# Performance work log

Measured on AMD Instinct MI355X. Metric: run time of the kernel, lower is better.

## Reference

```python
import jax, jax.numpy as jnp
import numpy as np

B, N, F_IN = 8, 1024, 128
C, E_FEAT, H = 128, 64, 4
E = 32768
NEG_SLOPE = 0.2


def setup_inputs() -> dict:
    key = jax.random.key(0)
    ks = jax.random.split(key, 7)
    return {
        "src": jax.random.normal(ks[0], (B, N, F_IN), dtype=jnp.float32),
        "edge_index": jax.random.randint(ks[1], (2, E), 0, N, dtype=jnp.int32),
        "W_lin": jax.random.normal(ks[2], (F_IN, C), dtype=jnp.float32) * (1.0 / np.sqrt(F_IN)),
        "a_src": jax.random.normal(ks[3], (C, H), dtype=jnp.float32) * (1.0 / np.sqrt(C)),
        "a_dst": jax.random.normal(ks[4], (C, H), dtype=jnp.float32) * (1.0 / np.sqrt(C)),
        "W_edge": jax.random.normal(ks[5], (F_IN, E_FEAT), dtype=jnp.float32) * (1.0 / np.sqrt(F_IN)),
        "a_edge": jax.random.normal(ks[6], (E_FEAT, H), dtype=jnp.float32) * (1.0 / np.sqrt(E_FEAT)),
    }


def reference(src, edge_index, W_lin, a_src, a_dst, W_edge, a_edge):
    # src: [B,N,F_in]; edge_index: [2,E]
    b, n, _ = src.shape
    h = a_src.shape[1]
    x = jnp.einsum("bnf,fc->bnc", src, W_lin)            # [B,N,C]
    attn_src = jnp.einsum("bnc,ch->bnh", x, a_src)        # [B,N,H]
    attn_dst = jnp.einsum("bnc,ch->bnh", x, a_dst)        # [B,N,H]
    # attn[b,i,j,h] = attn_src[b,i,h] + attn_dst[b,j,h]
    attn = attn_src[:, :, None, :] + attn_dst[:, None, :, :]  # [B,N,N,H]
    # edge term: (src_i - src_j) -> lin_edge -> a_edge, scattered into dense [B,N,N,H]
    diff = src[:, edge_index[0], :] - src[:, edge_index[1], :]    # [B,E,F_in]
    evals = jnp.einsum("bef,fd,dh->beh", diff, W_edge, a_edge)    # [B,E,H]
    edge_dense = jnp.zeros((b, n, n, h), src.dtype).at[:, edge_index[0], edge_index[1], :].add(evals)
    attn = jax.nn.leaky_relu(attn + edge_dense, NEG_SLOPE)
    # source applies softmax over the last dim (heads), faithful to nn.Softmax(dim=-1)
    return jax.nn.softmax(attn, axis=-1)
```

## Files before the change

kernel.cpp:

```cpp
#include <hip/hip_runtime.h>

#define B_SZ 8
#define N_SZ 1024
#define F_IN 128
#define C_DIM 128
#define E_FEAT 64
#define H_SZ 4
#define E_NUM 32768
#define NEG_SLOPE 0.2f


__global__ __launch_bounds__(256) void fold_mats(
    const float* __restrict__ W_lin, const float* __restrict__ a_src,
    const float* __restrict__ a_dst, const float* __restrict__ W_edge,
    const float* __restrict__ a_edge,
    float* __restrict__ m_src, float* __restrict__ m_dst,
    float* __restrict__ m_edge) {
  int idx = blockIdx.x * blockDim.x + threadIdx.x;
  if (idx >= F_IN * H_SZ) return;
  int f = idx >> 2, h = idx & 3;
  float accs = 0.f, accd = 0.f;
  for (int c = 0; c < C_DIM; ++c) {
    float w = W_lin[f * C_DIM + c];
    accs += w * a_src[c * H_SZ + h];
    accd += w * a_dst[c * H_SZ + h];
  }
  float acce = 0.f;
  for (int d = 0; d < E_FEAT; ++d)
    acce += W_edge[f * E_FEAT + d] * a_edge[d * H_SZ + h];
  m_src[idx] = accs; m_dst[idx] = accd; m_edge[idx] = acce;
}

__global__ __launch_bounds__(256) void node_vecs(
    const float* __restrict__ src, const float* __restrict__ m_src,
    const float* __restrict__ m_dst, const float* __restrict__ m_edge,
    float* __restrict__ as_, float* __restrict__ ad_, float* __restrict__ sw_) {
  int tid = blockIdx.x * blockDim.x + threadIdx.x;
  int h = tid & 3;
  int bn = tid >> 2;
  const float* row = src + (size_t)bn * F_IN;
  float a = 0.f, d = 0.f, e = 0.f;
  for (int f = 0; f < F_IN; ++f) {
    float s = row[f];
    a += s * m_src[f * H_SZ + h];
    d += s * m_dst[f * H_SZ + h];
    e += s * m_edge[f * H_SZ + h];
  }
  as_[tid] = a; ad_[tid] = d; sw_[tid] = e;
}

__global__ __launch_bounds__(256) void count_edges(
    const int* __restrict__ ei, int* __restrict__ cnt) {
  int e = blockIdx.x * blockDim.x + threadIdx.x;
  if (e < E_NUM) atomicAdd(&cnt[ei[e]], 1);
}

__global__ __launch_bounds__(1024) void scan_counts(
    const int* __restrict__ cnt, int* __restrict__ excl,
    int* __restrict__ cursor) {
  __shared__ int s[N_SZ];
  int t = threadIdx.x;
  int v0 = cnt[t];
  s[t] = v0;
  __syncthreads();
  for (int d = 1; d < N_SZ; d <<= 1) {
    int v = (t >= d) ? s[t - d] : 0;
    __syncthreads();
    s[t] += v;
    __syncthreads();
  }
  int ex = s[t] - v0;
  excl[t] = ex;
  cursor[t] = ex;
}

__global__ __launch_bounds__(256) void fill_edges(
    const int* __restrict__ ei, int* __restrict__ cursor,
    int* __restrict__ ebuf) {
  int e = blockIdx.x * blockDim.x + threadIdx.x;
  if (e >= E_NUM) return;
  int i = ei[e];
  int j = ei[E_NUM + e];
  int pos = atomicAdd(&cursor[i], 1);
  ebuf[pos] = j;
}

__global__ __launch_bounds__(256) void attn_main(
    const float* __restrict__ as_, const float* __restrict__ ad_,
    const float* __restrict__ sw_, const int* __restrict__ cnt,
    const int* __restrict__ excl, const int* __restrict__ ebuf,
    float* __restrict__ out) {
  __shared__ float row[N_SZ * H_SZ];
  int i = blockIdx.x, b = blockIdx.y, t = threadIdx.x;

  float4* row4 = (float4*)row;
  for (int k = t; k < N_SZ; k += 256) row4[k] = make_float4(0.f, 0.f, 0.f, 0.f);

  const float4* sw4 = (const float4*)sw_;
  float4 swi = sw4[b * N_SZ + i];
  float4 asi = ((const float4*)as_)[b * N_SZ + i];
  __syncthreads();

  int off = excl[i], c = cnt[i];
  for (int k = t; k < c; k += 256) {
    int j = ebuf[off + k];
    float4 swj = sw4[b * N_SZ + j];
    atomicAdd(&row[j * 4 + 0], swi.x - swj.x);
    atomicAdd(&row[j * 4 + 1], swi.y - swj.y);
    atomicAdd(&row[j * 4 + 2], swi.z - swj.z);
    atomicAdd(&row[j * 4 + 3], swi.w - swj.w);
  }
  __syncthreads();

  const float4* ad4 = (const float4*)ad_;
  float4* out4 = (float4*)out + (size_t)(b * N_SZ + i) * N_SZ;
#pragma unroll
  for (int r = 0; r < 4; ++r) {
    int j = r * 256 + t;
    float4 adj = ad4[b * N_SZ + j];
    float4 rv = row4[j];
    float v0 = asi.x + adj.x + rv.x;
    float v1 = asi.y + adj.y + rv.y;
    float v2 = asi.z + adj.z + rv.z;
    float v3 = asi.w + adj.w + rv.w;
    v0 = v0 > 0.f ? v0 : v0 * NEG_SLOPE;
    v1 = v1 > 0.f ? v1 : v1 * NEG_SLOPE;
    v2 = v2 > 0.f ? v2 : v2 * NEG_SLOPE;
    v3 = v3 > 0.f ? v3 : v3 * NEG_SLOPE;
    float m = fmaxf(fmaxf(v0, v1), fmaxf(v2, v3));
    float e0 = __expf(v0 - m);
    float e1 = __expf(v1 - m);
    float e2 = __expf(v2 - m);
    float e3 = __expf(v3 - m);
    float inv = 1.f / (e0 + e1 + e2 + e3);
    out4[j] = make_float4(e0 * inv, e1 * inv, e2 * inv, e3 * inv);
  }
}

extern "C" void kernel_launch(void* const* d_in, const int* in_sizes, int n_in,
                              void* d_out, int out_size, void* d_ws,
                              size_t ws_size, hipStream_t stream) {
  const float* src    = (const float*)d_in[0];
  const int*   ei     = (const int*)d_in[1];
  const float* W_lin  = (const float*)d_in[2];
  const float* a_src  = (const float*)d_in[3];
  const float* a_dst  = (const float*)d_in[4];
  const float* W_edge = (const float*)d_in[5];
  const float* a_edge = (const float*)d_in[6];
  float* out = (float*)d_out;

  float* ws     = (float*)d_ws;
  float* m_src  = ws;
  float* m_dst  = ws + 512;
  float* m_edge = ws + 1024;
  float* as_    = ws + 1536;
  float* ad_    = as_ + B_SZ * N_SZ * H_SZ;
  float* sw_    = ad_ + B_SZ * N_SZ * H_SZ;
  int*   cnt    = (int*)(sw_ + B_SZ * N_SZ * H_SZ);
  int*   excl   = cnt + N_SZ;
  int*   cursor = excl + N_SZ;
  int*   ebuf   = cursor + N_SZ;

  hipMemsetAsync(cnt, 0, N_SZ * sizeof(int), stream);
  count_edges<<<E_NUM / 256, 256, 0, stream>>>(ei, cnt);
  scan_counts<<<1, 1024, 0, stream>>>(cnt, excl, cursor);
  fill_edges<<<E_NUM / 256, 256, 0, stream>>>(ei, cursor, ebuf);
  fold_mats<<<2, 256, 0, stream>>>(W_lin, a_src, a_dst, W_edge, a_edge,
                                   m_src, m_dst, m_edge);
  node_vecs<<<B_SZ * N_SZ * H_SZ / 256, 256, 0, stream>>>(
      src, m_src, m_dst, m_edge, as_, ad_, sw_);
  attn_main<<<dim3(N_SZ, B_SZ), 256, 0, stream>>>(as_, ad_, sw_, cnt, excl,
                                                  ebuf, out);
}
```

Baseline: 190.3 us.

## Fuse prep kernels, warp-reduce node projections, seed row with ad, nontemporal stores

Folds the memset, edge count, scan, fill and fold-matrix launches into one two-block prep kernel that uses shared-memory atomics, cutting launch count from seven to three. The node projection kernel now has one wavefront per row and reduces with shuffles instead of a serial per-thread loop. The attention kernel seeds its shared row with ad instead of zeros, which removes a global load in the epilogue, and writes output with nontemporal stores. The cost is that the edge CSR build now runs serially in a single block.

```diff
diff --git a/kernel.cpp b/kernel.cpp
--- a/kernel.cpp
+++ b/kernel.cpp
@@ -9,80 +9,102 @@
 #define E_NUM 32768
 #define NEG_SLOPE 0.2f
 
+typedef float f4_t __attribute__((ext_vector_type(4)));
 
-__global__ __launch_bounds__(256) void fold_mats(
-    const float* __restrict__ W_lin, const float* __restrict__ a_src,
-    const float* __restrict__ a_dst, const float* __restrict__ W_edge,
-    const float* __restrict__ a_edge,
+
+__global__ __launch_bounds__(1024) void prep_kernel(
+    const int* __restrict__ ei, const float* __restrict__ W_lin,
+    const float* __restrict__ a_src, const float* __restrict__ a_dst,
+    const float* __restrict__ W_edge, const float* __restrict__ a_edge,
     float* __restrict__ m_src, float* __restrict__ m_dst,
-    float* __restrict__ m_edge) {
-  int idx = blockIdx.x * blockDim.x + threadIdx.x;
-  if (idx >= F_IN * H_SZ) return;
-  int f = idx >> 2, h = idx & 3;
-  float accs = 0.f, accd = 0.f;
-  for (int c = 0; c < C_DIM; ++c) {
-    float w = W_lin[f * C_DIM + c];
-    accs += w * a_src[c * H_SZ + h];
-    accd += w * a_dst[c * H_SZ + h];
+    float* __restrict__ m_edge, int* __restrict__ cnt_g,
+    int* __restrict__ excl_g, int* __restrict__ ebuf) {
+  if (blockIdx.x == 0) {
+    __shared__ int cntS[N_SZ];
+    __shared__ int s[N_SZ];
+    __shared__ int cur[N_SZ];
+    int t = threadIdx.x;
+    cntS[t] = 0;
+    __syncthreads();
+    for (int e = t; e < E_NUM; e += 1024) atomicAdd(&cntS[ei[e]], 1);
+    __syncthreads();
+    int v0 = cntS[t];
+    s[t] = v0;
+    __syncthreads();
+    for (int d2 = 1; d2 < N_SZ; d2 <<= 1) {
+      int v = (t >= d2) ? s[t - d2] : 0;
+      __syncthreads();
+      s[t] += v;
+      __syncthreads();
+    }
+    int ex = s[t] - v0;
+    cnt_g[t] = v0;
+    excl_g[t] = ex;
+    cur[t] = ex;
+    __syncthreads();
+    for (int e = t; e < E_NUM; e += 1024) {
+      int i = ei[e];
+      int j = ei[E_NUM + e];
+      int pos = atomicAdd(&cur[i], 1);
+      ebuf[pos] = j;
+    }
+  } else {
+    int idx = threadIdx.x;
+    if (idx >= F_IN * H_SZ) return;
+    int f = idx >> 2, h = idx & 3;
+    float accs = 0.f, accd = 0.f;
+    for (int c = 0; c < C_DIM; ++c) {
+      float w = W_lin[f * C_DIM + c];
+      accs += w * a_src[c * H_SZ + h];
+      accd += w * a_dst[c * H_SZ + h];
+    }
+    float acce = 0.f;
+    for (int d = 0; d < E_FEAT; ++d)
+      acce += W_edge[f * E_FEAT + d] * a_edge[d * H_SZ + h];
+    m_src[idx] = accs;
+    m_dst[idx] = accd;
+    m_edge[idx] = acce;
   }
-  float acce = 0.f;
-  for (int d = 0; d < E_FEAT; ++d)
-    acce += W_edge[f * E_FEAT + d] * a_edge[d * H_SZ + h];
-  m_src[idx] = accs; m_dst[idx] = accd; m_edge[idx] = acce;
 }
 
-__global__ __launch_bounds__(256) void node_vecs(
+__global__ __launch_bounds__(256) void nodes_kernel(
     const float* __restrict__ src, const float* __restrict__ m_src,
     const float* __restrict__ m_dst, const float* __restrict__ m_edge,
     float* __restrict__ as_, float* __restrict__ ad_, float* __restrict__ sw_) {
-  int tid = blockIdx.x * blockDim.x + threadIdx.x;
-  int h = tid & 3;
-  int bn = tid >> 2;
-  const float* row = src + (size_t)bn * F_IN;
-  float a = 0.f, d = 0.f, e = 0.f;
-  for (int f = 0; f < F_IN; ++f) {
-    float s = row[f];
-    a += s * m_src[f * H_SZ + h];
-    d += s * m_dst[f * H_SZ + h];
-    e += s * m_edge[f * H_SZ + h];
+  int wid = threadIdx.x >> 6, lane = threadIdx.x & 63;
+  int rid = blockIdx.x * 4 + wid;
+  const float* rp = src + (size_t)rid * F_IN;
+  float x0 = rp[lane];
+  float x1 = rp[lane + 64];
+  const float4* ms4 = (const float4*)m_src;
+  const float4* md4 = (const float4*)m_dst;
+  const float4* me4 = (const float4*)m_edge;
+  float4 s0 = ms4[lane], s1 = ms4[lane + 64];
+  float4 d0 = md4[lane], d1 = md4[lane + 64];
+  float4 e0 = me4[lane], e1 = me4[lane + 64];
+  float acc[12];
+  acc[0] = x0 * s0.x + x1 * s1.x;
+  acc[1] = x0 * s0.y + x1 * s1.y;
+  acc[2] = x0 * s0.z + x1 * s1.z;
+  acc[3] = x0 * s0.w + x1 * s1.w;
+  acc[4] = x0 * d0.x + x1 * d1.x;
+  acc[5] = x0 * d0.y + x1 * d1.y;
+  acc[6] = x0 * d0.z + x1 * d1.z;
+  acc[7] = x0 * d0.w + x1 * d1.w;
+  acc[8] = x0 * e0.x + x1 * e1.x;
+  acc[9] = x0 * e0.y + x1 * e1.y;
+  acc[10] = x0 * e0.z + x1 * e1.z;
+  acc[11] = x0 * e0.w + x1 * e1.w;
+#pragma unroll
+  for (int m = 1; m < 64; m <<= 1) {
+#pragma unroll
+    for (int q = 0; q < 12; ++q) acc[q] += __shfl_xor(acc[q], m);
   }
-  as_[tid] = a; ad_[tid] = d; sw_[tid] = e;
-}
-
-__global__ __launch_bounds__(256) void count_edges(
-    const int* __restrict__ ei, int* __restrict__ cnt) {
-  int e = blockIdx.x * blockDim.x + threadIdx.x;
-  if (e < E_NUM) atomicAdd(&cnt[ei[e]], 1);
-}
-
-__global__ __launch_bounds__(1024) void scan_counts(
-    const int* __restrict__ cnt, int* __restrict__ excl,
-    int* __restrict__ cursor) {
-  __shared__ int s[N_SZ];
-  int t = threadIdx.x;
-  int v0 = cnt[t];
-  s[t] = v0;
-  __syncthreads();
-  for (int d = 1; d < N_SZ; d <<= 1) {
-    int v = (t >= d) ? s[t - d] : 0;
-    __syncthreads();
-    s[t] += v;
-    __syncthreads();
+  if (lane == 0) {
+    ((float4*)as_)[rid] = make_float4(acc[0], acc[1], acc[2], acc[3]);
+    ((float4*)ad_)[rid] = make_float4(acc[4], acc[5], acc[6], acc[7]);
+    ((float4*)sw_)[rid] = make_float4(acc[8], acc[9], acc[10], acc[11]);
   }
-  int ex = s[t] - v0;
-  excl[t] = ex;
-  cursor[t] = ex;
-}
-
-__global__ __launch_bounds__(256) void fill_edges(
-    const int* __restrict__ ei, int* __restrict__ cursor,
-    int* __restrict__ ebuf) {
-  int e = blockIdx.x * blockDim.x + threadIdx.x;
-  if (e >= E_NUM) return;
-  int i = ei[e];
-  int j = ei[E_NUM + e];
-  int pos = atomicAdd(&cursor[i], 1);
-  ebuf[pos] = j;
 }
 
 __global__ __launch_bounds__(256) void attn_main(
@@ -92,19 +114,21 @@
     float* __restrict__ out) {
   __shared__ float row[N_SZ * H_SZ];
   int i = blockIdx.x, b = blockIdx.y, t = threadIdx.x;
+  int bN = b * N_SZ;
 
   float4* row4 = (float4*)row;
-  for (int k = t; k < N_SZ; k += 256) row4[k] = make_float4(0.f, 0.f, 0.f, 0.f);
+  const float4* ad4 = (const float4*)ad_;
+  const float4* sw4 = (const float4*)sw_;
+  for (int j = t; j < N_SZ; j += 256) row4[j] = ad4[bN + j];
 
-  const float4* sw4 = (const float4*)sw_;
-  float4 swi = sw4[b * N_SZ + i];
-  float4 asi = ((const float4*)as_)[b * N_SZ + i];
+  float4 swi = sw4[bN + i];
+  float4 asi = ((const float4*)as_)[bN + i];
   __syncthreads();
 
   int off = excl[i], c = cnt[i];
   for (int k = t; k < c; k += 256) {
     int j = ebuf[off + k];
-    float4 swj = sw4[b * N_SZ + j];
+    float4 swj = sw4[bN + j];
     atomicAdd(&row[j * 4 + 0], swi.x - swj.x);
     atomicAdd(&row[j * 4 + 1], swi.y - swj.y);
     atomicAdd(&row[j * 4 + 2], swi.z - swj.z);
@@ -112,28 +136,31 @@
   }
   __syncthreads();
 
-  const float4* ad4 = (const float4*)ad_;
-  float4* out4 = (float4*)out + (size_t)(b * N_SZ + i) * N_SZ;
+  f4_t* out4 = (f4_t*)out + (size_t)(bN + i) * N_SZ;
 #pragma unroll
   for (int r = 0; r < 4; ++r) {
     int j = r * 256 + t;
-    float4 adj = ad4[b * N_SZ + j];
     float4 rv = row4[j];
-    float v0 = asi.x + adj.x + rv.x;
-    float v1 = asi.y + adj.y + rv.y;
-    float v2 = asi.z + adj.z + rv.z;
-    float v3 = asi.w + adj.w + rv.w;
+    float v0 = asi.x + rv.x;
+    float v1 = asi.y + rv.y;
+    float v2 = asi.z + rv.z;
+    float v3 = asi.w + rv.w;
     v0 = v0 > 0.f ? v0 : v0 * NEG_SLOPE;
     v1 = v1 > 0.f ? v1 : v1 * NEG_SLOPE;
     v2 = v2 > 0.f ? v2 : v2 * NEG_SLOPE;
     v3 = v3 > 0.f ? v3 : v3 * NEG_SLOPE;
     float m = fmaxf(fmaxf(v0, v1), fmaxf(v2, v3));
-    float e0 = __expf(v0 - m);
-    float e1 = __expf(v1 - m);
-    float e2 = __expf(v2 - m);
-    float e3 = __expf(v3 - m);
-    float inv = 1.f / (e0 + e1 + e2 + e3);
-    out4[j] = make_float4(e0 * inv, e1 * inv, e2 * inv, e3 * inv);
+    float ex0 = __expf(v0 - m);
+    float ex1 = __expf(v1 - m);
+    float ex2 = __expf(v2 - m);
+    float ex3 = __expf(v3 - m);
+    float inv = 1.f / (ex0 + ex1 + ex2 + ex3);
+    f4_t o;
+    o.x = ex0 * inv;
+    o.y = ex1 * inv;
+    o.z = ex2 * inv;
+    o.w = ex3 * inv;
+    __builtin_nontemporal_store(o, &out4[j]);
   }
 }
 
@@ -158,17 +185,12 @@
   float* sw_    = ad_ + B_SZ * N_SZ * H_SZ;
   int*   cnt    = (int*)(sw_ + B_SZ * N_SZ * H_SZ);
   int*   excl   = cnt + N_SZ;
-  int*   cursor = excl + N_SZ;
-  int*   ebuf   = cursor + N_SZ;
+  int*   ebuf   = excl + N_SZ;
 
-  hipMemsetAsync(cnt, 0, N_SZ * sizeof(int), stream);
-  count_edges<<<E_NUM / 256, 256, 0, stream>>>(ei, cnt);
-  scan_counts<<<1, 1024, 0, stream>>>(cnt, excl, cursor);
-  fill_edges<<<E_NUM / 256, 256, 0, stream>>>(ei, cursor, ebuf);
-  fold_mats<<<2, 256, 0, stream>>>(W_lin, a_src, a_dst, W_edge, a_edge,
-                                   m_src, m_dst, m_edge);
-  node_vecs<<<B_SZ * N_SZ * H_SZ / 256, 256, 0, stream>>>(
-      src, m_src, m_dst, m_edge, as_, ad_, sw_);
+  prep_kernel<<<2, 1024, 0, stream>>>(ei, W_lin, a_src, a_dst, W_edge, a_edge,
+                                      m_src, m_dst, m_edge, cnt, excl, ebuf);
+  nodes_kernel<<<B_SZ * N_SZ / 4, 256, 0, stream>>>(src, m_src, m_dst, m_edge,
+                                                    as_, ad_, sw_);
   attn_main<<<dim3(N_SZ, B_SZ), 256, 0, stream>>>(as_, ad_, sw_, cnt, excl,
                                                   ebuf, out);
 }
```

Result: slower. 227.9 us (+19.7%).
